# Optimization experiments

Measured on AMD Instinct MI355X. Metric: run time of the kernel, lower is better.

Reference implementation:

```python
import jax, jax.numpy as jnp
import numpy as np

D_MODEL, H, D_FF = 1024, 16, 4096
D_K = D_MODEL // H
EPS = 1e-6
NEG = -1e9

def _layernorm(x, alpha, bias):
    # matches custom LayerNorm: unbiased std (torch default), scalar alpha/bias, divide by (std+eps)
    mean = jnp.mean(x, axis=-1, keepdims=True)
    std = jnp.std(x, axis=-1, keepdims=True, ddof=1)
    return alpha * ((x - mean) / (std + EPS)) + bias

def setup_inputs() -> dict:
    key = jax.random.key(0)
    ks = jax.random.split(key, 16)
    s = 0.02
    d = {
        'X': jax.random.normal(ks[0], (8, 1024, D_MODEL), dtype=jnp.float32),
        'mask': jnp.ones((8, 1, 1, 1024), dtype=jnp.int32),
        'wq': jax.random.normal(ks[1], (D_MODEL, D_MODEL), dtype=jnp.float32) * s,
        'bq': jnp.zeros((D_MODEL,), jnp.float32),
        'wk': jax.random.normal(ks[2], (D_MODEL, D_MODEL), dtype=jnp.float32) * s,
        'bk': jnp.zeros((D_MODEL,), jnp.float32),
        'wv': jax.random.normal(ks[3], (D_MODEL, D_MODEL), dtype=jnp.float32) * s,
        'bv': jnp.zeros((D_MODEL,), jnp.float32),
        'wo': jax.random.normal(ks[4], (D_MODEL, D_MODEL), dtype=jnp.float32) * s,
        'bo': jnp.zeros((D_MODEL,), jnp.float32),
        'w1': jax.random.normal(ks[5], (D_FF, D_MODEL), dtype=jnp.float32) * s,
        'b1': jnp.zeros((D_FF,), jnp.float32),
        'w2': jax.random.normal(ks[6], (D_MODEL, D_FF), dtype=jnp.float32) * s,
        'b2': jnp.zeros((D_MODEL,), jnp.float32),
        'ln1_a': jnp.ones((1,), jnp.float32), 'ln1_b': jnp.zeros((1,), jnp.float32),
        'ln2_a': jnp.ones((1,), jnp.float32), 'ln2_b': jnp.zeros((1,), jnp.float32),
    }
    return d

def reference(X, mask, wq, bq, wk, bk, wv, bv, wo, bo, w1, b1, w2, b2, ln1_a, ln1_b, ln2_a, ln2_b):
    B, S, _ = X.shape
    # --- self-attention sublayer (pre-norm residual); dropout = identity (eval) ---
    xn = _layernorm(X, ln1_a, ln1_b)
    q = (xn @ wq.T + bq).reshape(B, S, H, D_K)
    k = (xn @ wk.T + bk).reshape(B, S, H, D_K)
    v = (xn @ wv.T + bv).reshape(B, S, H, D_K)
    scores = jnp.einsum('bqhd,bkhd->bhqk', q, k) / jnp.sqrt(jnp.float32(D_K))
    scores = jnp.where(mask == 0, NEG, scores)
    attn = jax.nn.softmax(scores, axis=-1)
    ctx = jnp.einsum('bhqk,bkhd->bqhd', attn, v).reshape(B, S, D_MODEL)
    X = X + (ctx @ wo.T + bo)
    # --- feedforward sublayer (pre-norm residual) ---
    xn = _layernorm(X, ln2_a, ln2_b)
    h = jax.nn.relu(xn @ w1.T + b1)
    X = X + (h @ w2.T + b2)
    return X
```

## Files before the change

kernel.cpp:

```cpp
#include <hip/hip_runtime.h>
#include <cstdint>
#include <cstddef>

typedef float f32x4 __attribute__((ext_vector_type(4)));
typedef short bf16x8 __attribute__((ext_vector_type(8)));

typedef __attribute__((address_space(1))) void void_g;
typedef __attribute__((address_space(3))) void void_l;

__device__ __forceinline__ void gld16(const void* g, void* l) {
  __builtin_amdgcn_global_load_lds((void_g*)g, (void_l*)l, 16, 0, 0);
}

__device__ __forceinline__ unsigned short f2b(float f) {
  union { float f; uint32_t u; } c; c.f = f;
  uint32_t u = c.u;
  return (unsigned short)((u + 0x7fffu + ((u >> 16) & 1u)) >> 16);
}

__device__ __forceinline__ uint32_t cvtpk(float lo, float hi) {
  uint32_t r;
  asm("v_cvt_pk_bf16_f32 %0, %1, %2" : "=v"(r) : "v"(lo), "v"(hi));
  return r;
}

__device__ __forceinline__ float exp2_fast(float x) {
  return __builtin_exp2f(x);
}

__global__ __launch_bounds__(256) void cast_all(const float* __restrict__ w1,
                                                const float* __restrict__ w2,
                                                const float* __restrict__ wq,
                                                const float* __restrict__ wk,
                                                const float* __restrict__ wv,
                                                const float* __restrict__ wo,
                                                unsigned short* __restrict__ d1,
                                                unsigned short* __restrict__ d2,
                                                unsigned short* __restrict__ dqk,
                                                unsigned short* __restrict__ dv,
                                                unsigned short* __restrict__ dod) {
  int blk = blockIdx.x;
  const float* s;
  unsigned short* d;
  int off;
  if (blk < 4096) { s = w1; d = d1; off = blk; }
  else if (blk < 8192) { s = w2; d = d2; off = blk - 4096; }
  else if (blk < 9216) { s = wq; d = dqk; off = blk - 8192; }
  else if (blk < 10240) { s = wk; d = dqk + (1 << 20); off = blk - 9216; }
  else if (blk < 11264) { s = wv; d = dv; off = blk - 10240; }
  else { s = wo; d = dod; off = blk - 11264; }
  int i = off * 256 + threadIdx.x;
  float4 v = ((const float4*)s)[i];
  ushort4 o;
  o.x = f2b(v.x); o.y = f2b(v.y); o.z = f2b(v.z); o.w = f2b(v.w);
  ((ushort4*)d)[i] = o;
}

__global__ __launch_bounds__(256) void ln_bf16(const float* __restrict__ X,
                                               unsigned short* __restrict__ out,
                                               const float* __restrict__ alpha,
                                               const float* __restrict__ beta) {
  int row = blockIdx.x;
  int tid = threadIdx.x;
  float4 v = ((const float4*)(X + (size_t)row * 1024))[tid];
  float s = v.x + v.y + v.z + v.w;
  float q = v.x * v.x + v.y * v.y + v.z * v.z + v.w * v.w;
#pragma unroll
  for (int m = 1; m < 64; m <<= 1) { s += __shfl_xor(s, m); q += __shfl_xor(q, m); }
  __shared__ float red[8];
  int wave = tid >> 6;
  if ((tid & 63) == 0) { red[wave] = s; red[4 + wave] = q; }
  __syncthreads();
  s = red[0] + red[1] + red[2] + red[3];
  q = red[4] + red[5] + red[6] + red[7];
  float mean = s * (1.0f / 1024.0f);
  float var = fmaxf((q - 1024.0f * mean * mean) * (1.0f / 1023.0f), 0.0f);
  float inv = alpha[0] / (sqrtf(var) + 1e-6f);
  float b = beta[0];
  ushort4 o;
  o.x = f2b((v.x - mean) * inv + b);
  o.y = f2b((v.y - mean) * inv + b);
  o.z = f2b((v.z - mean) * inv + b);
  o.w = f2b((v.w - mean) * inv + b);
  ((ushort4*)(out + (size_t)row * 1024))[tid] = o;
}

template <int RELU, int BIAS2>
__global__ __launch_bounds__(512, 1) void gemm256(const unsigned short* __restrict__ A,
                                                  const unsigned short* __restrict__ W,
                                                  const float* __restrict__ bias,
                                                  const float* __restrict__ bias2, int b2off,
                                                  unsigned short* __restrict__ outB,
                                                  int M, int N, int K, int sA, int sW) {
  __shared__ unsigned short lds[2][4][128 * 64];
  int nbn = N >> 8;
  int nwg = gridDim.x;
  int bid = blockIdx.x;
  int wg = (bid & 7) * (nwg >> 3) + (bid >> 3);
  int tm = wg / nbn, tn = wg % nbn;
  int tid = threadIdx.x;
  int wave = tid >> 6, lane = tid & 63;
  int wr = wave >> 2, wc = wave & 3;
  int l15 = lane & 15, g = lane >> 4;
  int nt = K >> 6;

  const unsigned short* Abase = A + (size_t)(tm * 256) * sA;
  const unsigned short* Wbase = W + (size_t)(tn * 256) * sW;
  int srow = tid >> 3;
  int schunk = (tid & 7) ^ (srow & 7);

  f32x4 acc[8][4] = {};
  bf16x8 afrA[2][2], afrB[2][2], bfr[2][4];

  auto stage = [&](int buf, int s, int kt) {
    const unsigned short* base = (s < 2) ? Abase : Wbase;
    int str = (s < 2) ? sA : sW;
    int rbase = (s & 1) * 128;
#pragma unroll
    for (int e = 0; e < 2; ++e) {
      gld16(base + (size_t)(rbase + srow + e * 64) * str + kt * 64 + schunk * 8,
            &lds[buf][s][wave * 512 + e * 4096]);
    }
  };
  auto readB = [&](int buf) {
    const unsigned short* Bh = &lds[buf][2 + (wc >> 1)][0];
#pragma unroll
    for (int kk = 0; kk < 2; ++kk)
#pragma unroll
      for (int j = 0; j < 4; ++j) {
        int br = (wc & 1) * 64 + j * 16 + l15;
        bfr[kk][j] = *(const bf16x8*)&Bh[br * 64 + (((kk * 4 + g) ^ (br & 7)) * 8)];
      }
  };
  auto readA = [&](bf16x8 (&dst)[2][2], int buf, int q) {
    const unsigned short* Ah = &lds[buf][wr][0];
#pragma unroll
    for (int kk = 0; kk < 2; ++kk)
#pragma unroll
      for (int ri = 0; ri < 2; ++ri) {
        int ar = q * 32 + ri * 16 + l15;
        dst[kk][ri] = *(const bf16x8*)&Ah[ar * 64 + (((kk * 4 + g) ^ (ar & 7)) * 8)];
      }
  };
  auto mfma16 = [&](bf16x8 (&af)[2][2], int q) {
    __builtin_amdgcn_s_setprio(1);
#pragma unroll
    for (int kk = 0; kk < 2; ++kk)
#pragma unroll
      for (int ri = 0; ri < 2; ++ri)
#pragma unroll
        for (int j = 0; j < 4; ++j)
          acc[q * 2 + ri][j] = __builtin_amdgcn_mfma_f32_16x16x32_bf16(
              af[kk][ri], bfr[kk][j], acc[q * 2 + ri][j], 0, 0, 0);
    __builtin_amdgcn_s_setprio(0);
  };

  stage(0, 2, 0); stage(0, 3, 0); stage(0, 0, 0); stage(0, 1, 0);
  stage(1, 2, 1); stage(1, 3, 1);
  asm volatile("s_waitcnt vmcnt(4)" ::: "memory");
  __builtin_amdgcn_s_barrier();

  for (int t = 0; t < nt; ++t) {
    int buf = t & 1;
    __builtin_amdgcn_sched_barrier(0);
    if (t + 1 < nt) stage(buf ^ 1, 0, t + 1);
    readB(buf);
    readA(afrA, buf, 0);
    readA(afrB, buf, 1);
    mfma16(afrA, 0);
    __builtin_amdgcn_s_barrier();
    __builtin_amdgcn_sched_barrier(0);
    if (t + 1 < nt) stage(buf ^ 1, 1, t + 1);
    readA(afrA, buf, 2);
    mfma16(afrB, 1);
    __builtin_amdgcn_s_barrier();
    __builtin_amdgcn_sched_barrier(0);
    if (t + 2 < nt) stage(buf, 2, t + 2);
    readA(afrB, buf, 3);
    mfma16(afrA, 2);
    __builtin_amdgcn_s_barrier();
    __builtin_amdgcn_sched_barrier(0);
    if (t + 2 < nt) stage(buf, 3, t + 2);
    mfma16(afrB, 3);
    if (t + 2 < nt) asm volatile("s_waitcnt vmcnt(4)" ::: "memory");
    else asm volatile("s_waitcnt vmcnt(0)" ::: "memory");
    __builtin_amdgcn_s_barrier();
  }

  int row0 = tm * 256 + wr * 128 + g * 4;
  int col0 = tn * 256 + wc * 64 + l15;
#pragma unroll
  for (int i = 0; i < 8; ++i) {
#pragma unroll
    for (int j = 0; j < 4; ++j) {
      int col = col0 + j * 16;
      float bb = (BIAS2 && col >= b2off) ? bias2[col - b2off] : bias[col];
#pragma unroll
      for (int r = 0; r < 4; ++r) {
        int row = row0 + i * 16 + r;
        float v = acc[i][j][r] + bb;
        if (RELU) v = fmaxf(v, 0.0f);
        outB[(size_t)row * N + col] = f2b(v);
      }
    }
  }
}

template <int MODE>
__global__ __launch_bounds__(512, 1) void gemm256x128(const unsigned short* __restrict__ A,
                                                      const unsigned short* __restrict__ W,
                                                      const float* __restrict__ bias,
                                                      const float* __restrict__ resid,
                                                      float* __restrict__ outF,
                                                      unsigned short* __restrict__ outB,
                                                      int M, int N, int K, int sA, int sW) {
  __shared__ unsigned short lds[2][3][128 * 64];
  int nbn = N >> 7;
  int nwg = gridDim.x;
  int bid = blockIdx.x;
  int wg = (bid & 7) * (nwg >> 3) + (bid >> 3);
  int tm = wg / nbn, tn = wg % nbn;
  int tid = threadIdx.x;
  int wave = tid >> 6, lane = tid & 63;
  int wr = wave >> 2, wc = wave & 3;
  int l15 = lane & 15, g = lane >> 4;
  int nt = K >> 6;

  const unsigned short* Abase = A + (size_t)(tm * 256) * sA;
  const unsigned short* Wbase = W + (size_t)(tn * 128) * sW;
  int srow = tid >> 3;
  int schunk = (tid & 7) ^ (srow & 7);

  f32x4 acc[8][2] = {};
  bf16x8 afrA[2][2], afrB[2][2], bfr[2][2];

  auto stage = [&](int buf, int s, int kt) {
    const unsigned short* base = (s < 2) ? Abase : Wbase;
    int str = (s < 2) ? sA : sW;
    int rbase = (s & 1) * 128;
#pragma unroll
    for (int e = 0; e < 2; ++e) {
      gld16(base + (size_t)(rbase + srow + e * 64) * str + kt * 64 + schunk * 8,
            &lds[buf][s][wave * 512 + e * 4096]);
    }
  };
  auto readB = [&](int buf) {
    const unsigned short* Bh = &lds[buf][2][0];
#pragma unroll
    for (int kk = 0; kk < 2; ++kk)
#pragma unroll
      for (int j = 0; j < 2; ++j) {
        int br = wc * 32 + j * 16 + l15;
        bfr[kk][j] = *(const bf16x8*)&Bh[br * 64 + (((kk * 4 + g) ^ (br & 7)) * 8)];
      }
  };
  auto readA = [&](bf16x8 (&dst)[2][2], int buf, int q) {
    const unsigned short* Ah = &lds[buf][wr][0];
#pragma unroll
    for (int kk = 0; kk < 2; ++kk)
#pragma unroll
      for (int ri = 0; ri < 2; ++ri) {
        int ar = q * 32 + ri * 16 + l15;
        dst[kk][ri] = *(const bf16x8*)&Ah[ar * 64 + (((kk * 4 + g) ^ (ar & 7)) * 8)];
      }
  };
  auto mfma8 = [&](bf16x8 (&af)[2][2], int q) {
    __builtin_amdgcn_s_setprio(1);
#pragma unroll
    for (int kk = 0; kk < 2; ++kk)
#pragma unroll
      for (int ri = 0; ri < 2; ++ri)
#pragma unroll
        for (int j = 0; j < 2; ++j)
          acc[q * 2 + ri][j] = __builtin_amdgcn_mfma_f32_16x16x32_bf16(
              af[kk][ri], bfr[kk][j], acc[q * 2 + ri][j], 0, 0, 0);
    __builtin_amdgcn_s_setprio(0);
  };

  stage(0, 2, 0); stage(0, 0, 0); stage(0, 1, 0);
  stage(1, 2, 1);
  asm volatile("s_waitcnt vmcnt(2)" ::: "memory");
  __builtin_amdgcn_s_barrier();

  for (int t = 0; t < nt; ++t) {
    int buf = t & 1;
    __builtin_amdgcn_sched_barrier(0);
    if (t + 1 < nt) stage(buf ^ 1, 0, t + 1);
    readB(buf);
    readA(afrA, buf, 0);
    readA(afrB, buf, 1);
    mfma8(afrA, 0);
    __builtin_amdgcn_s_barrier();
    __builtin_amdgcn_sched_barrier(0);
    if (t + 1 < nt) stage(buf ^ 1, 1, t + 1);
    readA(afrA, buf, 2);
    mfma8(afrB, 1);
    __builtin_amdgcn_s_barrier();
    __builtin_amdgcn_sched_barrier(0);
    if (t + 2 < nt) stage(buf, 2, t + 2);
    readA(afrB, buf, 3);
    mfma8(afrA, 2);
    __builtin_amdgcn_s_barrier();
    __builtin_amdgcn_sched_barrier(0);
    mfma8(afrB, 3);
    if (t + 2 < nt) asm volatile("s_waitcnt vmcnt(2)" ::: "memory");
    else asm volatile("s_waitcnt vmcnt(0)" ::: "memory");
    __builtin_amdgcn_s_barrier();
  }

  int row0 = tm * 256 + wr * 128 + g * 4;
  int col0 = tn * 128 + wc * 32 + l15;
#pragma unroll
  for (int i = 0; i < 8; ++i) {
#pragma unroll
    for (int j = 0; j < 2; ++j) {
      int col = col0 + j * 16;
      float cb = (MODE == 2) ? bias[col] : 0.0f;
#pragma unroll
      for (int r = 0; r < 4; ++r) {
        int row = row0 + i * 16 + r;
        size_t idx = (size_t)row * N + col;
        float v = acc[i][j][r];
        if (MODE == 1) outB[idx] = f2b(v + bias[row]);
        else if (MODE == 2) outF[idx] = resid[idx] + v + cb;
        else outF[idx] += v;
      }
    }
  }
}

__global__ __launch_bounds__(256) void attn_fwd6(const unsigned short* __restrict__ QK,
                                                 const unsigned short* __restrict__ Vt,
                                                 const int* __restrict__ mask,
                                                 unsigned short* __restrict__ O) {
  __shared__ unsigned short Kl[2][64 * 64];
  __shared__ unsigned short Vl[2][64 * 64];
  __shared__ float biasl[1024];
  int bid = blockIdx.x;
  int wg = (bid & 7) * 128 + (bid >> 3);
  int qt = wg & 7, bh = wg >> 3;
  int b = bh >> 4, h = bh & 15;
  int tid = threadIdx.x, wave = tid >> 6, lane = tid & 63;
  int l15 = lane & 15, g = lane >> 4;
  int q0 = qt * 128;

  for (int i = tid; i < 1024; i += 256)
    biasl[i] = (mask[b * 1024 + i] == 0) ? -1.4426950e9f : 0.0f;

  const unsigned short* QrowA = QK + ((size_t)(b * 1024 + q0 + wave * 16 + l15)) * 2048 + h * 64;
  const unsigned short* QrowB = QrowA + (size_t)64 * 2048;
  bf16x8 qa0 = *(const bf16x8*)(QrowA + g * 8);
  bf16x8 qa1 = *(const bf16x8*)(QrowA + 32 + g * 8);
  bf16x8 qb0 = *(const bf16x8*)(QrowB + g * 8);
  bf16x8 qb1 = *(const bf16x8*)(QrowB + 32 + g * 8);

  float l_a = 0.0f, l_b = 0.0f;
  f32x4 oa[4] = {}, ob[4] = {};

  int srow = lane >> 3;
  int clog = (lane & 7) ^ srow;
  int h7 = l15 & 7;
  const float SC = 0.125f * 1.44269504f;

  auto stageKV = [&](int buf, int kt) {
#pragma unroll
    for (int i = 0; i < 2; ++i) {
      int rk = wave * 16 + i * 8 + srow;
      gld16(QK + ((size_t)(b * 1024 + kt * 64 + rk)) * 2048 + 1024 + h * 64 + clog * 8,
            &Kl[buf][(wave * 16 + i * 8) * 64]);
      gld16(Vt + ((size_t)(h * 64 + rk)) * 8192 + b * 1024 + kt * 64 + clog * 8,
            &Vl[buf][(wave * 16 + i * 8) * 64]);
    }
  };

  stageKV(0, 0);
  __syncthreads();
  int cur = 0;

  for (int kt = 0; kt < 16; ++kt) {
    if (kt < 15) stageKV(cur ^ 1, kt + 1);

    f32x4 sa[4], sb[4];
    __builtin_amdgcn_s_setprio(1);
#pragma unroll
    for (int j = 0; j < 4; ++j) {
      int kr = j * 16 + l15;
      bf16x8 ka = *(const bf16x8*)&Kl[cur][kr * 64 + ((g ^ h7) * 8)];
      bf16x8 kb = *(const bf16x8*)&Kl[cur][kr * 64 + (((4 + g) ^ h7) * 8)];
      f32x4 z = {};
      sa[j] = __builtin_amdgcn_mfma_f32_16x16x32_bf16(ka, qa0, z, 0, 0, 0);
      sa[j] = __builtin_amdgcn_mfma_f32_16x16x32_bf16(kb, qa1, sa[j], 0, 0, 0);
      sb[j] = __builtin_amdgcn_mfma_f32_16x16x32_bf16(ka, qb0, z, 0, 0, 0);
      sb[j] = __builtin_amdgcn_mfma_f32_16x16x32_bf16(kb, qb1, sb[j], 0, 0, 0);
    }
    __builtin_amdgcn_s_setprio(0);

    union U8 { uint32_t u[4]; bf16x8 v; } pa[2], pb[2];
#pragma unroll
    for (int j = 0; j < 4; ++j) {
      float4 b4 = *(const float4*)&biasl[kt * 64 + j * 16 + g * 4];
      float ea0 = exp2_fast(sa[j][0] * SC + b4.x);
      float ea1 = exp2_fast(sa[j][1] * SC + b4.y);
      float ea2 = exp2_fast(sa[j][2] * SC + b4.z);
      float ea3 = exp2_fast(sa[j][3] * SC + b4.w);
      l_a += (ea0 + ea1) + (ea2 + ea3);
      pa[j >> 1].u[(j & 1) * 2 + 0] = cvtpk(ea0, ea1);
      pa[j >> 1].u[(j & 1) * 2 + 1] = cvtpk(ea2, ea3);
      float eb0 = exp2_fast(sb[j][0] * SC + b4.x);
      float eb1 = exp2_fast(sb[j][1] * SC + b4.y);
      float eb2 = exp2_fast(sb[j][2] * SC + b4.z);
      float eb3 = exp2_fast(sb[j][3] * SC + b4.w);
      l_b += (eb0 + eb1) + (eb2 + eb3);
      pb[j >> 1].u[(j & 1) * 2 + 0] = cvtpk(eb0, eb1);
      pb[j >> 1].u[(j & 1) * 2 + 1] = cvtpk(eb2, eb3);
    }

    __builtin_amdgcn_s_setprio(1);
#pragma unroll
    for (int kk = 0; kk < 2; ++kk) {
#pragma unroll
      for (int dt = 0; dt < 4; ++dt) {
        int vr = dt * 16 + l15;
        uint2 lo = *(const uint2*)&Vl[cur][vr * 64 + (((4 * kk + (g >> 1)) ^ h7) * 8) + (g & 1) * 4];
        uint2 hi = *(const uint2*)&Vl[cur][vr * 64 + (((4 * kk + 2 + (g >> 1)) ^ h7) * 8) + (g & 1) * 4];
        union U8 vbu;
        vbu.u[0] = lo.x; vbu.u[1] = lo.y; vbu.u[2] = hi.x; vbu.u[3] = hi.y;
        oa[dt] = __builtin_amdgcn_mfma_f32_16x16x32_bf16(vbu.v, pa[kk].v, oa[dt], 0, 0, 0);
        ob[dt] = __builtin_amdgcn_mfma_f32_16x16x32_bf16(vbu.v, pb[kk].v, ob[dt], 0, 0, 0);
      }
    }
    __builtin_amdgcn_s_setprio(0);

    __syncthreads();
    cur ^= 1;
  }

  l_a += __shfl_xor(l_a, 16);
  l_a += __shfl_xor(l_a, 32);
  l_b += __shfl_xor(l_b, 16);
  l_b += __shfl_xor(l_b, 32);
  float inva = 1.0f / l_a, invb = 1.0f / l_b;
  size_t orowA = ((size_t)(b * 1024 + q0 + wave * 16 + l15)) * 1024 + h * 64;
  size_t orowB = orowA + (size_t)64 * 1024;
#pragma unroll
  for (int dt = 0; dt < 4; ++dt) {
    uint2 wa, wb;
    wa.x = cvtpk(oa[dt][0] * inva, oa[dt][1] * inva);
    wa.y = cvtpk(oa[dt][2] * inva, oa[dt][3] * inva);
    *(uint2*)&O[orowA + dt * 16 + g * 4] = wa;
    wb.x = cvtpk(ob[dt][0] * invb, ob[dt][1] * invb);
    wb.y = cvtpk(ob[dt][2] * invb, ob[dt][3] * invb);
    *(uint2*)&O[orowB + dt * 16 + g * 4] = wb;
  }
}

extern "C" void kernel_launch(void* const* d_in, const int* in_sizes, int n_in,
                              void* d_out, int out_size, void* d_ws, size_t ws_size,
                              hipStream_t stream) {
  const float* X = (const float*)d_in[0];
  const int* mask = (const int*)d_in[1];
  const float* wq = (const float*)d_in[2];
  const float* bq = (const float*)d_in[3];
  const float* wk = (const float*)d_in[4];
  const float* bk = (const float*)d_in[5];
  const float* wv = (const float*)d_in[6];
  const float* bv = (const float*)d_in[7];
  const float* wo = (const float*)d_in[8];
  const float* bo = (const float*)d_in[9];
  const float* w1 = (const float*)d_in[10];
  const float* b1 = (const float*)d_in[11];
  const float* w2 = (const float*)d_in[12];
  const float* b2 = (const float*)d_in[13];
  const float* ln1a = (const float*)d_in[14];
  const float* ln1b = (const float*)d_in[15];
  const float* ln2a = (const float*)d_in[16];
  const float* ln2b = (const float*)d_in[17];
  float* out = (float*)d_out;
  char* ws = (char*)d_ws;
  const size_t MB = 1024 * 1024;

  unsigned short* w1_b = (unsigned short*)(ws + 0 * MB);
  unsigned short* w2_b = (unsigned short*)(ws + 8 * MB);
  unsigned short* wqk_b = (unsigned short*)(ws + 16 * MB);
  unsigned short* wv_b = (unsigned short*)(ws + 20 * MB);
  unsigned short* wo_b = (unsigned short*)(ws + 22 * MB);
  unsigned short* xn = (unsigned short*)(ws + 24 * MB);
  unsigned short* QKb = (unsigned short*)(ws + 40 * MB);
  unsigned short* Vtb = (unsigned short*)(ws + 72 * MB);
  unsigned short* hb = QKb;

  cast_all<<<12288, 256, 0, stream>>>(w1, w2, wq, wk, wv, wo, w1_b, w2_b, wqk_b, wv_b, wo_b);

  ln_bf16<<<8192, 256, 0, stream>>>(X, xn, ln1a, ln1b);
  gemm256<0, 1><<<256, 512, 0, stream>>>(xn, wqk_b, bq, bk, 1024, QKb,
                                         8192, 2048, 1024, 1024, 1024);
  gemm256x128<1><<<256, 512, 0, stream>>>(wv_b, xn, bv, nullptr, nullptr, Vtb,
                                          1024, 8192, 1024, 1024, 1024);
  attn_fwd6<<<1024, 256, 0, stream>>>(QKb, Vtb, mask, xn);
  gemm256x128<2><<<256, 512, 0, stream>>>(xn, wo_b, bo, X, out, nullptr,
                                          8192, 1024, 1024, 1024, 1024);
  ln_bf16<<<8192, 256, 0, stream>>>(out, xn, ln2a, ln2b);
  for (int hc = 0; hc < 2; ++hc) {
    gemm256<1, 0><<<256, 512, 0, stream>>>(xn, w1_b + (size_t)hc * 2048 * 1024,
                                           b1 + hc * 2048, nullptr, 0, hb,
                                           8192, 2048, 1024, 1024, 1024);
    if (hc == 0)
      gemm256x128<2><<<256, 512, 0, stream>>>(hb, w2_b, b2, out, out, nullptr,
                                              8192, 1024, 2048, 2048, 4096);
    else
      gemm256x128<3><<<256, 512, 0, stream>>>(hb, w2_b + 2048, nullptr, nullptr, out, nullptr,
                                              8192, 1024, 2048, 2048, 4096);
  }
}
```

Before: 359.7 us.

## Split attention query tile across eight waves with one row block each

The attention kernel now runs 512 threads per block, and each of the eight waves owns 16 query rows instead of four waves each owning two 16-row blocks. K/V staging is spread over all 512 threads, one global-to-LDS load per thread per buffer. This halves per-wave registers and MFMA work and raises wave-level parallelism and occupancy (launch bounds 512, 6). In exchange, each wave reads the K/V LDS tiles for only 16 rows, so LDS read traffic per output doubles.

```diff
diff --git a/kernel.cpp b/kernel.cpp
--- a/kernel.cpp
+++ b/kernel.cpp
@@ -329,10 +329,10 @@
   }
 }
 
-__global__ __launch_bounds__(256) void attn_fwd6(const unsigned short* __restrict__ QK,
-                                                 const unsigned short* __restrict__ Vt,
-                                                 const int* __restrict__ mask,
-                                                 unsigned short* __restrict__ O) {
+__global__ __launch_bounds__(512, 6) void attn_fwd7(const unsigned short* __restrict__ QK,
+                                                    const unsigned short* __restrict__ Vt,
+                                                    const int* __restrict__ mask,
+                                                    unsigned short* __restrict__ O) {
   __shared__ unsigned short Kl[2][64 * 64];
   __shared__ unsigned short Vl[2][64 * 64];
   __shared__ float biasl[1024];
@@ -344,33 +344,26 @@
   int l15 = lane & 15, g = lane >> 4;
   int q0 = qt * 128;
 
-  for (int i = tid; i < 1024; i += 256)
+  for (int i = tid; i < 1024; i += 512)
     biasl[i] = (mask[b * 1024 + i] == 0) ? -1.4426950e9f : 0.0f;
 
-  const unsigned short* QrowA = QK + ((size_t)(b * 1024 + q0 + wave * 16 + l15)) * 2048 + h * 64;
-  const unsigned short* QrowB = QrowA + (size_t)64 * 2048;
-  bf16x8 qa0 = *(const bf16x8*)(QrowA + g * 8);
-  bf16x8 qa1 = *(const bf16x8*)(QrowA + 32 + g * 8);
-  bf16x8 qb0 = *(const bf16x8*)(QrowB + g * 8);
-  bf16x8 qb1 = *(const bf16x8*)(QrowB + 32 + g * 8);
-
-  float l_a = 0.0f, l_b = 0.0f;
-  f32x4 oa[4] = {}, ob[4] = {};
-
-  int srow = lane >> 3;
-  int clog = (lane & 7) ^ srow;
+  const unsigned short* Qrow = QK + ((size_t)(b * 1024 + q0 + wave * 16 + l15)) * 2048 + h * 64;
+  bf16x8 qf0 = *(const bf16x8*)(Qrow + g * 8);
+  bf16x8 qf1 = *(const bf16x8*)(Qrow + 32 + g * 8);
+
+  float l_q = 0.0f;
+  f32x4 o[4] = {};
+
+  int srow = tid >> 3;
+  int clog = (tid & 7) ^ (srow & 7);
   int h7 = l15 & 7;
   const float SC = 0.125f * 1.44269504f;
 
   auto stageKV = [&](int buf, int kt) {
-#pragma unroll
-    for (int i = 0; i < 2; ++i) {
-      int rk = wave * 16 + i * 8 + srow;
-      gld16(QK + ((size_t)(b * 1024 + kt * 64 + rk)) * 2048 + 1024 + h * 64 + clog * 8,
-            &Kl[buf][(wave * 16 + i * 8) * 64]);
-      gld16(Vt + ((size_t)(h * 64 + rk)) * 8192 + b * 1024 + kt * 64 + clog * 8,
-            &Vl[buf][(wave * 16 + i * 8) * 64]);
-    }
+    gld16(QK + ((size_t)(b * 1024 + kt * 64 + srow)) * 2048 + 1024 + h * 64 + clog * 8,
+          &Kl[buf][(wave * 8) * 64]);
+    gld16(Vt + ((size_t)(h * 64 + srow)) * 8192 + b * 1024 + kt * 64 + clog * 8,
+          &Vl[buf][(wave * 8) * 64]);
   };
 
   stageKV(0, 0);
@@ -380,7 +373,7 @@
   for (int kt = 0; kt < 16; ++kt) {
     if (kt < 15) stageKV(cur ^ 1, kt + 1);
 
-    f32x4 sa[4], sb[4];
+    f32x4 st[4];
     __builtin_amdgcn_s_setprio(1);
 #pragma unroll
     for (int j = 0; j < 4; ++j) {
@@ -388,31 +381,22 @@
       bf16x8 ka = *(const bf16x8*)&Kl[cur][kr * 64 + ((g ^ h7) * 8)];
       bf16x8 kb = *(const bf16x8*)&Kl[cur][kr * 64 + (((4 + g) ^ h7) * 8)];
       f32x4 z = {};
-      sa[j] = __builtin_amdgcn_mfma_f32_16x16x32_bf16(ka, qa0, z, 0, 0, 0);
-      sa[j] = __builtin_amdgcn_mfma_f32_16x16x32_bf16(kb, qa1, sa[j], 0, 0, 0);
-      sb[j] = __builtin_amdgcn_mfma_f32_16x16x32_bf16(ka, qb0, z, 0, 0, 0);
-      sb[j] = __builtin_amdgcn_mfma_f32_16x16x32_bf16(kb, qb1, sb[j], 0, 0, 0);
+      st[j] = __builtin_amdgcn_mfma_f32_16x16x32_bf16(ka, qf0, z, 0, 0, 0);
+      st[j] = __builtin_amdgcn_mfma_f32_16x16x32_bf16(kb, qf1, st[j], 0, 0, 0);
     }
     __builtin_amdgcn_s_setprio(0);
 
-    union U8 { uint32_t u[4]; bf16x8 v; } pa[2], pb[2];
+    union U8 { uint32_t u[4]; bf16x8 v; } pa[2];
 #pragma unroll
     for (int j = 0; j < 4; ++j) {
       float4 b4 = *(const float4*)&biasl[kt * 64 + j * 16 + g * 4];
-      float ea0 = exp2_fast(sa[j][0] * SC + b4.x);
-      float ea1 = exp2_fast(sa[j][1] * SC + b4.y);
-      float ea2 = exp2_fast(sa[j][2] * SC + b4.z);
-      float ea3 = exp2_fast(sa[j][3] * SC + b4.w);
-      l_a += (ea0 + ea1) + (ea2 + ea3);
-      pa[j >> 1].u[(j & 1) * 2 + 0] = cvtpk(ea0, ea1);
-      pa[j >> 1].u[(j & 1) * 2 + 1] = cvtpk(ea2, ea3);
-      float eb0 = exp2_fast(sb[j][0] * SC + b4.x);
-      float eb1 = exp2_fast(sb[j][1] * SC + b4.y);
-      float eb2 = exp2_fast(sb[j][2] * SC + b4.z);
-      float eb3 = exp2_fast(sb[j][3] * SC + b4.w);
-      l_b += (eb0 + eb1) + (eb2 + eb3);
-      pb[j >> 1].u[(j & 1) * 2 + 0] = cvtpk(eb0, eb1);
-      pb[j >> 1].u[(j & 1) * 2 + 1] = cvtpk(eb2, eb3);
+      float e0 = exp2_fast(st[j][0] * SC + b4.x);
+      float e1 = exp2_fast(st[j][1] * SC + b4.y);
+      float e2 = exp2_fast(st[j][2] * SC + b4.z);
+      float e3 = exp2_fast(st[j][3] * SC + b4.w);
+      l_q += (e0 + e1) + (e2 + e3);
+      pa[j >> 1].u[(j & 1) * 2 + 0] = cvtpk(e0, e1);
+      pa[j >> 1].u[(j & 1) * 2 + 1] = cvtpk(e2, e3);
     }
 
     __builtin_amdgcn_s_setprio(1);
@@ -425,8 +409,7 @@
         uint2 hi = *(const uint2*)&Vl[cur][vr * 64 + (((4 * kk + 2 + (g >> 1)) ^ h7) * 8) + (g & 1) * 4];
         union U8 vbu;
         vbu.u[0] = lo.x; vbu.u[1] = lo.y; vbu.u[2] = hi.x; vbu.u[3] = hi.y;
-        oa[dt] = __builtin_amdgcn_mfma_f32_16x16x32_bf16(vbu.v, pa[kk].v, oa[dt], 0, 0, 0);
-        ob[dt] = __builtin_amdgcn_mfma_f32_16x16x32_bf16(vbu.v, pb[kk].v, ob[dt], 0, 0, 0);
+        o[dt] = __builtin_amdgcn_mfma_f32_16x16x32_bf16(vbu.v, pa[kk].v, o[dt], 0, 0, 0);
       }
     }
     __builtin_amdgcn_s_setprio(0);
@@ -435,22 +418,16 @@
     cur ^= 1;
   }
 
-  l_a += __shfl_xor(l_a, 16);
-  l_a += __shfl_xor(l_a, 32);
-  l_b += __shfl_xor(l_b, 16);
-  l_b += __shfl_xor(l_b, 32);
-  float inva = 1.0f / l_a, invb = 1.0f / l_b;
-  size_t orowA = ((size_t)(b * 1024 + q0 + wave * 16 + l15)) * 1024 + h * 64;
-  size_t orowB = orowA + (size_t)64 * 1024;
+  l_q += __shfl_xor(l_q, 16);
+  l_q += __shfl_xor(l_q, 32);
+  float inv = 1.0f / l_q;
+  size_t orow = ((size_t)(b * 1024 + q0 + wave * 16 + l15)) * 1024 + h * 64;
 #pragma unroll
   for (int dt = 0; dt < 4; ++dt) {
-    uint2 wa, wb;
-    wa.x = cvtpk(oa[dt][0] * inva, oa[dt][1] * inva);
-    wa.y = cvtpk(oa[dt][2] * inva, oa[dt][3] * inva);
-    *(uint2*)&O[orowA + dt * 16 + g * 4] = wa;
-    wb.x = cvtpk(ob[dt][0] * invb, ob[dt][1] * invb);
-    wb.y = cvtpk(ob[dt][2] * invb, ob[dt][3] * invb);
-    *(uint2*)&O[orowB + dt * 16 + g * 4] = wb;
+    uint2 w;
+    w.x = cvtpk(o[dt][0] * inv, o[dt][1] * inv);
+    w.y = cvtpk(o[dt][2] * inv, o[dt][3] * inv);
+    *(uint2*)&O[orow + dt * 16 + g * 4] = w;
   }
 }
 
@@ -496,7 +473,7 @@
                                          8192, 2048, 1024, 1024, 1024);
   gemm256x128<1><<<256, 512, 0, stream>>>(wv_b, xn, bv, nullptr, nullptr, Vtb,
                                           1024, 8192, 1024, 1024, 1024);
-  attn_fwd6<<<1024, 256, 0, stream>>>(QKb, Vtb, mask, xn);
+  attn_fwd7<<<1024, 512, 0, stream>>>(QKb, Vtb, mask, xn);
   gemm256x128<2><<<256, 512, 0, stream>>>(xn, wo_b, bo, X, out, nullptr,
                                           8192, 1024, 1024, 1024, 1024);
   ln_bf16<<<8192, 256, 0, stream>>>(out, xn, ln2a, ln2b);
```

New measurement: 358.8 us. About the same (-0.2%).
